# Kernel optimization log

Hardware: AMD Instinct MI355X
Metric: run time of the kernel (lower is better)

Reference implementation:

```python
import jax, jax.numpy as jnp
import numpy as np

B, C, L, HEADS, DK = 32, 128, 32, 8, 64  # batch, channels, lattice side (L1=L2=L), heads, head dim
NLAYER = 4


def setup_inputs() -> dict:
    key = jax.random.key(0)
    ks = jax.random.split(key, 6)
    s_in = 1.0 / float(np.sqrt(C))          # lecun-normal scale for QKV (fan_in = channels)
    s_out = 1.0 / float(np.sqrt(HEADS * DK))  # lecun-normal scale for W0 (fan_in = dk*heads)
    return {
        "x": jax.random.normal(ks[0], (B, C, L, L), jnp.float32),
        "Wq": jax.random.normal(ks[1], (HEADS * DK, C), jnp.float32) * s_in,
        "Wk": jax.random.normal(ks[2], (HEADS * DK, C), jnp.float32) * s_in,
        "Wv": jax.random.normal(ks[3], (HEADS * DK, C), jnp.float32) * s_in,
        "R": jax.random.normal(ks[4], (HEADS, L, L), jnp.float32) * 0.02,
        "W0": jax.random.normal(ks[5], (C, HEADS * DK), jnp.float32) * s_out,
    }


def get_irpe(R):
    # r[h, i, j] = R[h, (xi - xj) mod L1, (yi - yj) mod L2]  (jnp negative indexing wraps)
    heads, L1, L2 = R.shape
    a1 = jnp.arange(L1)
    a2 = jnp.arange(L2)
    dx = (a1[:, None] - a1[None, :]) % L1        # (L1, L1)
    dy = (a2[:, None] - a2[None, :]) % L2        # (L2, L2)
    bias = R[:, dx[:, None, :, None], dy[None, :, None, :]]  # (heads, L1, L2, L1, L2)
    return bias.reshape(heads, L1 * L2, L1 * L2)


def reference(x, Wq, Wk, Wv, R, W0):
    bias = get_irpe(R)                            # (heads, N, N)
    inv_layer = 1.0 / float(np.sqrt(NLAYER + 1))
    inv_sqrt_dk = 1.0 / float(np.sqrt(DK))

    def block(xs):  # xs: (C, L, L) — single sample, as in the original __call__
        xn = xs * inv_layer
        xf = xn.reshape(C, -1)                    # (C, N)
        Q = (Wq @ xf).reshape(HEADS, DK, -1)      # 1x1 conv == matmul
        K = (Wk @ xf).reshape(HEADS, DK, -1)
        V = (Wv @ xf).reshape(HEADS, DK, -1)
        dot = jnp.einsum('hdi,hdj->hij', Q, K) + bias
        alpha = jax.nn.softmax(dot * inv_sqrt_dk, axis=-1)
        att = jnp.einsum('hij,hdj->hdi', alpha, V).reshape(HEADS * DK, -1)
        return (W0 @ att).reshape(xs.shape) + xs  # residual

    return jax.vmap(block)(x)
```

## Files before the change

### kernel.cpp

```cpp
#include <hip/hip_runtime.h>


#define NB   32
#define NH   8
#define SEQ  1024
#define DKH  64
#define HDIM 512
#define CIN  128

#define SCL 0.18033688011112042f

typedef __bf16 bf16x8 __attribute__((ext_vector_type(8)));
typedef float floatx4 __attribute__((ext_vector_type(4)));
typedef unsigned short u16x8 __attribute__((ext_vector_type(8)));
typedef unsigned int uintx4 __attribute__((ext_vector_type(4)));

__device__ __forceinline__ unsigned short f2bf(float f) {
    union { float f; unsigned int u; } c; c.f = f;
    unsigned int u = c.u;
    return (unsigned short)((u + 0x7fffu + ((u >> 16) & 1u)) >> 16);
}
__device__ __forceinline__ bf16x8 ldfrag(const unsigned short* p) {
    u16x8 v = *reinterpret_cast<const u16x8*>(p);
    return __builtin_bit_cast(bf16x8, v);
}
__device__ __forceinline__ unsigned int pkbf(float a, float b) {
    unsigned int ua = __builtin_bit_cast(unsigned int, a);
    unsigned int ub = __builtin_bit_cast(unsigned int, b);
    ua += 0x7fffu + ((ua >> 16) & 1u);
    ub += 0x7fffu + ((ub >> 16) & 1u);
    return __builtin_amdgcn_perm(ub, ua, 0x07060302u);
}
__device__ __forceinline__ unsigned int pkbf_t(float a, float b) {
    return __builtin_amdgcn_perm(__builtin_bit_cast(unsigned int, b),
                                 __builtin_bit_cast(unsigned int, a), 0x07060302u);
}


__global__ __launch_bounds__(256) void prep_wb(const float* __restrict__ Wq,
                                               const float* __restrict__ Wk,
                                               const float* __restrict__ Wv,
                                               const float* __restrict__ W0,
                                               const float* __restrict__ R,
                                               unsigned short* __restrict__ w2,
                                               unsigned short* __restrict__ w0f,
                                               float* __restrict__ biasG) {
    if (blockIdx.x < 256) {
        int gidx = blockIdx.x * 256 + threadIdx.x;
        int lane = gidx & 63, slot = gidx >> 6;
        int bb = slot & 1, a = (slot >> 1) & 1, dxx = (slot >> 2) & 31, h = slot >> 7;
        int q = lane >> 4, n = lane & 15;
        int iy = (a << 4) + n;
        const float* Rh = R + (h << 10) + (dxx << 5);
        floatx4 v;
        for (int r = 0; r < 4; ++r) {
            int jy = (bb << 4) + 4 * q + r;
            v[r] = Rh[(iy - jy) & 31] * SCL;
        }
        *(floatx4*)&biasG[(size_t)gidx * 4] = v;
    } else {
        int idx = (blockIdx.x - 256) * 256 + threadIdx.x;
        if (idx < 196608) {
            int row = idx >> 7, col = idx & 127;
            float v;
            if (row < 512)       v = Wq[idx] * SCL;
            else if (row < 1024) v = Wk[idx - 65536];
            else                 v = Wv[idx - 131072];
            int rt = row >> 4, nr = row & 15, kc = col >> 5, qc = (col & 31) >> 3, jc = col & 7;
            w2[((rt * 4 + kc) * 512) + (qc * 16 + nr) * 8 + jc] = f2bf(v);
        } else {
            int idx2 = idx - 196608;
            int row = idx2 >> 9, col = idx2 & 511;
            int rt = row >> 4, nr = row & 15, kcA = col >> 5, qc = (col & 31) >> 3, jc = col & 7;
            w0f[((rt * 16 + kcA) * 512) + (qc * 16 + nr) * 8 + jc] = f2bf(W0[idx2]);
        }
    }
}

__global__ __launch_bounds__(256) void prep_xt(const float* __restrict__ x,
                                               unsigned short* __restrict__ xt2) {
    __shared__ float lds[64 * 65];
    int b = blockIdx.x, c0 = blockIdx.y * 64, p0 = blockIdx.z * 64;
    int t = threadIdx.x, tr = t >> 6, tc = t & 63;
    const float inv_layer = 0.44721359549995793f;
    for (int rr = 0; rr < 16; ++rr) {
        int cl = rr * 4 + tr;
        lds[cl * 65 + tc] = x[(b * CIN + c0 + cl) * SEQ + p0 + tc];
    }
    __syncthreads();
    for (int rr = 0; rr < 16; ++rr) {
        int pl = rr * 4 + tr;
        int pos = p0 + pl, c = c0 + tc;
        int pt = pos >> 4, np = pos & 15, kc = c >> 5, qc = (c & 31) >> 3, jc = c & 7;
        xt2[((size_t)((b * 64 + pt) * 4 + kc) * 512) + (qc * 16 + np) * 8 + jc] =
            f2bf(lds[tc * 65 + pl] * inv_layer);
    }
}

__global__ __launch_bounds__(256, 4) void qkv_gemm(const unsigned short* __restrict__ xt2,
                                                   const unsigned short* __restrict__ w2,
                                                   unsigned short* __restrict__ Qt,
                                                   unsigned short* __restrict__ Kf,
                                                   unsigned short* __restrict__ Vf) {
    int b = blockIdx.x, y = blockIdx.y, zt = blockIdx.z;
    int tid = threadIdx.x, wave = tid >> 6, lane = tid & 63, q = lane >> 4, n = lane & 15;
    floatx4 acc[4];
    for (int s = 0; s < 4; ++s) acc[s] = (floatx4){0.f, 0.f, 0.f, 0.f};
    bf16x8 af[4], bfr[4][4];
    if (y < 16) {
        int rt = y * 4 + wave;
        const unsigned short* wbase = w2 + (size_t)rt * 4 * 512 + lane * 8;
        const unsigned short* xbase = xt2 + (size_t)(b * 64 + zt * 4) * 4 * 512 + lane * 8;
        for (int kc = 0; kc < 4; ++kc) af[kc] = ldfrag(wbase + kc * 512);
        for (int s = 0; s < 4; ++s)
            for (int kc = 0; kc < 4; ++kc) bfr[s][kc] = ldfrag(xbase + (s * 4 + kc) * 512);
        for (int kc = 0; kc < 4; ++kc)
            for (int s = 0; s < 4; ++s)
                acc[s] = __builtin_amdgcn_mfma_f32_16x16x32_bf16(af[kc], bfr[s][kc], acc[s], 0, 0, 0);
        int wrow0 = y * 64 + wave * 16;
        int pos0 = zt * 64;
        if (y < 8) {
            int h = wrow0 >> 6;
            int d0 = (wrow0 & 63) + 4 * q;
            for (int s = 0; s < 4; ++s) {
                uint2 pk;
                pk.x = pkbf(acc[s][0], acc[s][1]);
                pk.y = pkbf(acc[s][2], acc[s][3]);
                int pos = pos0 + 16 * s + n;
                *(uint2*)&Qt[((size_t)(b * NH + h) * SEQ + pos) * DKH + d0] = pk;
            }
        } else {
            int h = (wrow0 >> 6) - 8;
            int bh = b * NH + h;
            int cd = wave >> 1;
            int qk = 2 * (wave & 1) + (q >> 1);
            int jk = 4 * (q & 1);
            for (int s = 0; s < 4; ++s) {
                uint2 pk;
                pk.x = pkbf(acc[s][0], acc[s][1]);
                pk.y = pkbf(acc[s][2], acc[s][3]);
                size_t addr = ((size_t)(bh * 16 + zt) * 8 + s * 2 + cd) * 512
                              + (qk * 16 + n) * 8 + jk;
                *(uint2*)&Kf[addr] = pk;
            }
        }
    } else {
        int pt = zt * 4 + wave;
        const unsigned short* xbase = xt2 + (size_t)((b * 64 + pt) * 4) * 512 + lane * 8;
        int rtv0 = 64 + (y - 16) * 4;
        const unsigned short* wbase = w2 + (size_t)rtv0 * 4 * 512 + lane * 8;
        for (int kc = 0; kc < 4; ++kc) af[kc] = ldfrag(xbase + kc * 512);
        for (int s = 0; s < 4; ++s)
            for (int kc = 0; kc < 4; ++kc) bfr[s][kc] = ldfrag(wbase + (s * 4 + kc) * 512);
        for (int kc = 0; kc < 4; ++kc)
            for (int s = 0; s < 4; ++s)
                acc[s] = __builtin_amdgcn_mfma_f32_16x16x32_bf16(af[kc], bfr[s][kc], acc[s], 0, 0, 0);
        int vrow0 = (y - 16) * 64;
        int cj = wave >> 1;
        int jj0 = 4 * (wave & 1);
        for (int s = 0; s < 4; ++s) {
            int vrow = vrow0 + 16 * s + n;
            int h = vrow >> 6, d = vrow & 63;
            int u = d >> 4, nl = d & 15;
            uint2 pk;
            pk.x = pkbf(acc[s][0], acc[s][1]);
            pk.y = pkbf(acc[s][2], acc[s][3]);
            size_t addr = ((size_t)((b * NH + h) * 16 + zt) * 8 + u * 2 + cj) * 512
                          + (q * 16 + nl) * 8 + jj0;
            *(uint2*)&Vf[addr] = pk;
        }
    }
}

__global__ __launch_bounds__(256, 2) void attn_kernel(const unsigned short* __restrict__ Qt,
                                                      const unsigned short* __restrict__ Kf,
                                                      const unsigned short* __restrict__ Vf,
                                                      const float* __restrict__ biasG,
                                                      unsigned short* __restrict__ att2) {
    __shared__ alignas(16) unsigned short lds_k[2][8 * 512];
    __shared__ alignas(16) unsigned short lds_v[2][8 * 512];

    int gid = blockIdx.x;
    int bh = gid & 255, qb = gid >> 8;
    int b = bh >> 3, h = bh & 7;
    int tid = threadIdx.x, wave = tid >> 6, lane = tid & 63, q = lane >> 4, n = lane & 15;
    int i0 = qb * 256 + wave * 64;
    int ti0 = i0 >> 4;

    const unsigned short* qbase = Qt + (size_t)bh * SEQ * DKH;
    const unsigned short* kft = Kf + (size_t)bh * 16 * 4096;
    const unsigned short* vft = Vf + (size_t)bh * 16 * 4096;
    const float* bGh = biasG + ((size_t)h * 32 * 4 * 256) + lane * 4;

    bf16x8 aq[4][2];
    for (int qt = 0; qt < 4; ++qt)
        for (int c = 0; c < 2; ++c)
            aq[qt][c] = ldfrag(qbase + (i0 + 16 * qt + n) * DKH + c * 32 + q * 8);

    u16x8 ones_u;
    for (int t = 0; t < 8; ++t) ones_u[t] = 0x3F80;
    bf16x8 vone = __builtin_bit_cast(bf16x8, ones_u);

    floatx4 o[4][4], acc_l[4];
    for (int qt = 0; qt < 4; ++qt) {
        acc_l[qt] = (floatx4){0.f, 0.f, 0.f, 0.f};
        for (int u = 0; u < 4; ++u) o[qt][u] = (floatx4){0.f, 0.f, 0.f, 0.f};
    }

    {
        const unsigned short* kp = kft + tid * 16;
        const unsigned short* vp = vft + tid * 16;
        u16x8 k0 = *(const u16x8*)kp, k1 = *(const u16x8*)(kp + 8);
        u16x8 v0 = *(const u16x8*)vp, v1 = *(const u16x8*)(vp + 8);
        *(u16x8*)&lds_k[0][tid * 16]     = k0;
        *(u16x8*)&lds_k[0][tid * 16 + 8] = k1;
        *(u16x8*)&lds_v[0][tid * 16]     = v0;
        *(u16x8*)&lds_v[0][tid * 16 + 8] = v1;
    }
    __syncthreads();

    for (int kt = 0; kt < 16; ++kt) {
        int cur = kt & 1;
        u16x8 kpre0, kpre1, vpre0, vpre1;
        if (kt < 15) {
            const unsigned short* kp = kft + (kt + 1) * 4096 + tid * 16;
            const unsigned short* vp = vft + (kt + 1) * 4096 + tid * 16;
            kpre0 = *(const u16x8*)kp;  kpre1 = *(const u16x8*)(kp + 8);
            vpre0 = *(const u16x8*)vp;  vpre1 = *(const u16x8*)(vp + 8);
        }

        floatx4 bsv[4][4];
        for (int qt = 0; qt < 4; ++qt) {
            int tq = ti0 + qt;
            int a512 = (tq & 1) << 9;
            int e0 = (tq >> 1) - 2 * kt;
            for (int s = 0; s < 4; ++s) {
                int dxx = (e0 - (s >> 1)) & 31;
                bsv[qt][s] = *(const floatx4*)(bGh + (dxx << 10) + a512 + ((s & 1) << 8));
            }
        }

        bf16x8 kf2[4][2];
        for (int s = 0; s < 4; ++s)
            for (int c = 0; c < 2; ++c)
                kf2[s][c] = ldfrag(&lds_k[cur][(s * 2 + c) * 512 + lane * 8]);

        bf16x8 pf[4][2];
        for (int qt = 0; qt < 4; ++qt) {
            floatx4 sv[4];
            for (int s = 0; s < 4; ++s) {
                sv[s] = __builtin_amdgcn_mfma_f32_16x16x32_bf16(kf2[s][0], aq[qt][0], bsv[qt][s], 0, 0, 0);
                sv[s] = __builtin_amdgcn_mfma_f32_16x16x32_bf16(kf2[s][1], aq[qt][1], sv[s], 0, 0, 0);
            }
            for (int c = 0; c < 2; ++c) {
                uintx4 pu;
                pu[0] = pkbf_t(__builtin_amdgcn_exp2f(sv[2 * c][0]), __builtin_amdgcn_exp2f(sv[2 * c][1]));
                pu[1] = pkbf_t(__builtin_amdgcn_exp2f(sv[2 * c][2]), __builtin_amdgcn_exp2f(sv[2 * c][3]));
                pu[2] = pkbf_t(__builtin_amdgcn_exp2f(sv[2 * c + 1][0]), __builtin_amdgcn_exp2f(sv[2 * c + 1][1]));
                pu[3] = pkbf_t(__builtin_amdgcn_exp2f(sv[2 * c + 1][2]), __builtin_amdgcn_exp2f(sv[2 * c + 1][3]));
                pf[qt][c] = __builtin_bit_cast(bf16x8, pu);
            }
        }

        bf16x8 vf2[4][2];
        for (int u = 0; u < 4; ++u)
            for (int c = 0; c < 2; ++c)
                vf2[u][c] = ldfrag(&lds_v[cur][(u * 2 + c) * 512 + lane * 8]);
        for (int qt = 0; qt < 4; ++qt) {
            acc_l[qt] = __builtin_amdgcn_mfma_f32_16x16x32_bf16(vone, pf[qt][0], acc_l[qt], 0, 0, 0);
            acc_l[qt] = __builtin_amdgcn_mfma_f32_16x16x32_bf16(vone, pf[qt][1], acc_l[qt], 0, 0, 0);
        }
        for (int u = 0; u < 4; ++u)
            for (int qt = 0; qt < 4; ++qt) {
                o[qt][u] = __builtin_amdgcn_mfma_f32_16x16x32_bf16(vf2[u][0], pf[qt][0], o[qt][u], 0, 0, 0);
                o[qt][u] = __builtin_amdgcn_mfma_f32_16x16x32_bf16(vf2[u][1], pf[qt][1], o[qt][u], 0, 0, 0);
            }

        if (kt < 15) {
            int nxt = cur ^ 1;
            *(u16x8*)&lds_k[nxt][tid * 16]     = kpre0;
            *(u16x8*)&lds_k[nxt][tid * 16 + 8] = kpre1;
            *(u16x8*)&lds_v[nxt][tid * 16]     = vpre0;
            *(u16x8*)&lds_v[nxt][tid * 16 + 8] = vpre1;
        }
        __syncthreads();
    }

    for (int qt = 0; qt < 4; ++qt) {
        float inv = 1.0f / acc_l[qt][0];
        int pt = ti0 + qt;
        for (int u = 0; u < 4; ++u) {
            int kcA = 2 * h + (u >> 1);
            int q2 = 2 * (u & 1) + (q >> 1);
            uint2 pk;
            pk.x = pkbf(o[qt][u][0] * inv, o[qt][u][1] * inv);
            pk.y = pkbf(o[qt][u][2] * inv, o[qt][u][3] * inv);
            size_t addr = ((size_t)((b * 64 + pt) * 16 + kcA) * 512)
                          + (q2 * 16 + n) * 8 + 4 * (q & 1);
            *(uint2*)&att2[addr] = pk;
        }
    }
}

__global__ __launch_bounds__(256, 4) void out_gemm(const unsigned short* __restrict__ att2,
                                                   const unsigned short* __restrict__ w0f,
                                                   const float* __restrict__ x,
                                                   float* __restrict__ out) {
    int b = blockIdx.x, ct = blockIdx.y, ptb = blockIdx.z;
    int tid = threadIdx.x, wave = tid >> 6, lane = tid & 63, q = lane >> 4, n = lane & 15;
    int pos0 = ptb * 64 + wave * 16;
    int c0 = ct * 64;
    int pt = ptb * 4 + wave;
    const unsigned short* abase = att2 + (size_t)(b * 64 + pt) * 16 * 512 + lane * 8;
    const unsigned short* wbase = w0f + (size_t)(c0 >> 4) * 16 * 512 + lane * 8;
    floatx4 acc[4];
    for (int s = 0; s < 4; ++s) acc[s] = (floatx4){0.f, 0.f, 0.f, 0.f};
    for (int g = 0; g < 4; ++g) {
        bf16x8 af[4], bfr[4][4];
        for (int k2 = 0; k2 < 4; ++k2) af[k2] = ldfrag(abase + (g * 4 + k2) * 512);
        for (int s = 0; s < 4; ++s)
            for (int k2 = 0; k2 < 4; ++k2)
                bfr[s][k2] = ldfrag(wbase + (s * 16 + g * 4 + k2) * 512);
        for (int k2 = 0; k2 < 4; ++k2)
            for (int s = 0; s < 4; ++s)
                acc[s] = __builtin_amdgcn_mfma_f32_16x16x32_bf16(af[k2], bfr[s][k2], acc[s], 0, 0, 0);
    }
    int p0q = pos0 + 4 * q;
    for (int s = 0; s < 4; ++s) {
        int c = c0 + 16 * s + n;
        size_t idx = ((size_t)b * CIN + c) * SEQ + p0q;
        floatx4 res = *(const floatx4*)&x[idx];
        floatx4 v = acc[s] + res;
        *(floatx4*)&out[idx] = v;
    }
}

extern "C" void kernel_launch(void* const* d_in, const int* in_sizes, int n_in,
                              void* d_out, int out_size, void* d_ws, size_t ws_size,
                              hipStream_t stream) {
    const float* x  = (const float*)d_in[0];
    const float* Wq = (const float*)d_in[1];
    const float* Wk = (const float*)d_in[2];
    const float* Wv = (const float*)d_in[3];
    const float* R  = (const float*)d_in[4];
    const float* W0 = (const float*)d_in[5];
    float* out = (float*)d_out;

    char* ws = (char*)d_ws;
    size_t off = 0;
    unsigned short* Qt   = (unsigned short*)(ws + off); off += (size_t)NB * NH * SEQ * DKH * 2;
    unsigned short* Kf   = (unsigned short*)(ws + off); off += (size_t)NB * NH * SEQ * DKH * 2;
    unsigned short* Vf   = (unsigned short*)(ws + off); off += (size_t)NB * NH * SEQ * DKH * 2;
    unsigned short* att2 = (unsigned short*)(ws + off); off += (size_t)NB * SEQ * HDIM * 2;
    unsigned short* xt2  = (unsigned short*)(ws + off); off += (size_t)NB * SEQ * CIN * 2;
    unsigned short* w2   = (unsigned short*)(ws + off); off += (size_t)1536 * 128 * 2;
    unsigned short* w0f  = (unsigned short*)(ws + off); off += (size_t)128 * 512 * 2;
    float* biasG = (float*)(ws + off); off += (size_t)NH * 32 * 4 * 256 * 4;
    (void)ws_size; (void)in_sizes; (void)n_in; (void)out_size;

    prep_wb<<<1280, 256, 0, stream>>>(Wq, Wk, Wv, W0, R, w2, w0f, biasG);
    prep_xt<<<dim3(NB, 2, 16), 256, 0, stream>>>(x, xt2);
    qkv_gemm<<<dim3(NB, 24, 16), 256, 0, stream>>>(xt2, w2, Qt, Kf, Vf);
    attn_kernel<<<NB * NH * 4, 256, 0, stream>>>(Qt, Kf, Vf, biasG, att2);
    out_gemm<<<dim3(NB, 2, 16), 256, 0, stream>>>(att2, w0f, x, out);
}
```

Measured before the change: 214.5 us.

## Use direct global-to-LDS loads and halve per-block query tile in attention

The attention kernel now streams K/V tiles into shared memory with global_load_lds DMA instead of staging them through registers, and drops the register prefetch copies. Each block handles 128 queries (32 per wave) instead of 256, doubling the grid and raising the occupancy target to 4 blocks per CU. Bias values are loaded inline per tile rather than batched up front. This cuts register pressure and raises parallelism, but every K/V tile is now reloaded by twice as many blocks, and there is a possible race on the DMA completing before the barrier.

New measurement: 230.9 us. +7.6%, slower.

```diff
diff --git a/kernel.cpp b/kernel.cpp
--- a/kernel.cpp
+++ b/kernel.cpp
@@ -34,6 +34,11 @@
 __device__ __forceinline__ unsigned int pkbf_t(float a, float b) {
     return __builtin_amdgcn_perm(__builtin_bit_cast(unsigned int, b),
                                  __builtin_bit_cast(unsigned int, a), 0x07060302u);
+}
+__device__ __forceinline__ void dma16(const unsigned short* g, unsigned short* l) {
+    __builtin_amdgcn_global_load_lds(
+        (const __attribute__((address_space(1))) unsigned int*)g,
+        (__attribute__((address_space(3))) unsigned int*)l, 16, 0, 0);
 }
 
 
@@ -172,7 +177,7 @@
     }
 }
 
-__global__ __launch_bounds__(256, 2) void attn_kernel(const unsigned short* __restrict__ Qt,
+__global__ __launch_bounds__(256, 4) void attn_kernel(const unsigned short* __restrict__ Qt,
                                                       const unsigned short* __restrict__ Kf,
                                                       const unsigned short* __restrict__ Vf,
                                                       const float* __restrict__ biasG,
@@ -184,7 +189,7 @@
     int bh = gid & 255, qb = gid >> 8;
     int b = bh >> 3, h = bh & 7;
     int tid = threadIdx.x, wave = tid >> 6, lane = tid & 63, q = lane >> 4, n = lane & 15;
-    int i0 = qb * 256 + wave * 64;
+    int i0 = qb * 128 + wave * 32;
     int ti0 = i0 >> 4;
 
     const unsigned short* qbase = Qt + (size_t)bh * SEQ * DKH;
@@ -192,8 +197,8 @@
     const unsigned short* vft = Vf + (size_t)bh * 16 * 4096;
     const float* bGh = biasG + ((size_t)h * 32 * 4 * 256) + lane * 4;
 
-    bf16x8 aq[4][2];
-    for (int qt = 0; qt < 4; ++qt)
+    bf16x8 aq[2][2];
+    for (int qt = 0; qt < 2; ++qt)
         for (int c = 0; c < 2; ++c)
             aq[qt][c] = ldfrag(qbase + (i0 + 16 * qt + n) * DKH + c * 32 + q * 8);
 
@@ -201,43 +206,29 @@
     for (int t = 0; t < 8; ++t) ones_u[t] = 0x3F80;
     bf16x8 vone = __builtin_bit_cast(bf16x8, ones_u);
 
-    floatx4 o[4][4], acc_l[4];
-    for (int qt = 0; qt < 4; ++qt) {
+    floatx4 o[2][4], acc_l[2];
+    for (int qt = 0; qt < 2; ++qt) {
         acc_l[qt] = (floatx4){0.f, 0.f, 0.f, 0.f};
         for (int u = 0; u < 4; ++u) o[qt][u] = (floatx4){0.f, 0.f, 0.f, 0.f};
     }
 
-    {
-        const unsigned short* kp = kft + tid * 16;
-        const unsigned short* vp = vft + tid * 16;
-        u16x8 k0 = *(const u16x8*)kp, k1 = *(const u16x8*)(kp + 8);
-        u16x8 v0 = *(const u16x8*)vp, v1 = *(const u16x8*)(vp + 8);
-        *(u16x8*)&lds_k[0][tid * 16]     = k0;
-        *(u16x8*)&lds_k[0][tid * 16 + 8] = k1;
-        *(u16x8*)&lds_v[0][tid * 16]     = v0;
-        *(u16x8*)&lds_v[0][tid * 16 + 8] = v1;
-    }
+    int sb = wave * 1024;
+    dma16(kft + sb + lane * 8,        &lds_k[0][sb]);
+    dma16(kft + sb + 512 + lane * 8,  &lds_k[0][sb + 512]);
+    dma16(vft + sb + lane * 8,        &lds_v[0][sb]);
+    dma16(vft + sb + 512 + lane * 8,  &lds_v[0][sb + 512]);
     __syncthreads();
 
     for (int kt = 0; kt < 16; ++kt) {
         int cur = kt & 1;
-        u16x8 kpre0, kpre1, vpre0, vpre1;
         if (kt < 15) {
-            const unsigned short* kp = kft + (kt + 1) * 4096 + tid * 16;
-            const unsigned short* vp = vft + (kt + 1) * 4096 + tid * 16;
-            kpre0 = *(const u16x8*)kp;  kpre1 = *(const u16x8*)(kp + 8);
-            vpre0 = *(const u16x8*)vp;  vpre1 = *(const u16x8*)(vp + 8);
-        }
-
-        floatx4 bsv[4][4];
-        for (int qt = 0; qt < 4; ++qt) {
-            int tq = ti0 + qt;
-            int a512 = (tq & 1) << 9;
-            int e0 = (tq >> 1) - 2 * kt;
-            for (int s = 0; s < 4; ++s) {
-                int dxx = (e0 - (s >> 1)) & 31;
-                bsv[qt][s] = *(const floatx4*)(bGh + (dxx << 10) + a512 + ((s & 1) << 8));
-            }
+            int nxt = cur ^ 1;
+            const unsigned short* kp = kft + (kt + 1) * 4096 + sb;
+            const unsigned short* vp = vft + (kt + 1) * 4096 + sb;
+            dma16(kp + lane * 8,       &lds_k[nxt][sb]);
+            dma16(kp + 512 + lane * 8, &lds_k[nxt][sb + 512]);
+            dma16(vp + lane * 8,       &lds_v[nxt][sb]);
+            dma16(vp + 512 + lane * 8, &lds_v[nxt][sb + 512]);
         }
 
         bf16x8 kf2[4][2];
@@ -245,11 +236,16 @@
             for (int c = 0; c < 2; ++c)
                 kf2[s][c] = ldfrag(&lds_k[cur][(s * 2 + c) * 512 + lane * 8]);
 
-        bf16x8 pf[4][2];
-        for (int qt = 0; qt < 4; ++qt) {
+        bf16x8 pf[2][2];
+        for (int qt = 0; qt < 2; ++qt) {
+            int tq = ti0 + qt;
+            int a512 = (tq & 1) << 9;
+            int e0 = (tq >> 1) - 2 * kt;
             floatx4 sv[4];
             for (int s = 0; s < 4; ++s) {
-                sv[s] = __builtin_amdgcn_mfma_f32_16x16x32_bf16(kf2[s][0], aq[qt][0], bsv[qt][s], 0, 0, 0);
+                int dxx = (e0 - (s >> 1)) & 31;
+                floatx4 bsv = *(const floatx4*)(bGh + (dxx << 10) + a512 + ((s & 1) << 8));
+                sv[s] = __builtin_amdgcn_mfma_f32_16x16x32_bf16(kf2[s][0], aq[qt][0], bsv, 0, 0, 0);
                 sv[s] = __builtin_amdgcn_mfma_f32_16x16x32_bf16(kf2[s][1], aq[qt][1], sv[s], 0, 0, 0);
             }
             for (int c = 0; c < 2; ++c) {
@@ -266,27 +262,20 @@
         for (int u = 0; u < 4; ++u)
             for (int c = 0; c < 2; ++c)
                 vf2[u][c] = ldfrag(&lds_v[cur][(u * 2 + c) * 512 + lane * 8]);
-        for (int qt = 0; qt < 4; ++qt) {
+        for (int qt = 0; qt < 2; ++qt) {
             acc_l[qt] = __builtin_amdgcn_mfma_f32_16x16x32_bf16(vone, pf[qt][0], acc_l[qt], 0, 0, 0);
             acc_l[qt] = __builtin_amdgcn_mfma_f32_16x16x32_bf16(vone, pf[qt][1], acc_l[qt], 0, 0, 0);
         }
         for (int u = 0; u < 4; ++u)
-            for (int qt = 0; qt < 4; ++qt) {
+            for (int qt = 0; qt < 2; ++qt) {
                 o[qt][u] = __builtin_amdgcn_mfma_f32_16x16x32_bf16(vf2[u][0], pf[qt][0], o[qt][u], 0, 0, 0);
                 o[qt][u] = __builtin_amdgcn_mfma_f32_16x16x32_bf16(vf2[u][1], pf[qt][1], o[qt][u], 0, 0, 0);
             }
 
-        if (kt < 15) {
-            int nxt = cur ^ 1;
-            *(u16x8*)&lds_k[nxt][tid * 16]     = kpre0;
-            *(u16x8*)&lds_k[nxt][tid * 16 + 8] = kpre1;
-            *(u16x8*)&lds_v[nxt][tid * 16]     = vpre0;
-            *(u16x8*)&lds_v[nxt][tid * 16 + 8] = vpre1;
-        }
         __syncthreads();
     }
 
-    for (int qt = 0; qt < 4; ++qt) {
+    for (int qt = 0; qt < 2; ++qt) {
         float inv = 1.0f / acc_l[qt][0];
         int pt = ti0 + qt;
         for (int u = 0; u < 4; ++u) {
@@ -361,6 +350,6 @@
     prep_wb<<<1280, 256, 0, stream>>>(Wq, Wk, Wv, W0, R, w2, w0f, biasG);
     prep_xt<<<dim3(NB, 2, 16), 256, 0, stream>>>(x, xt2);
     qkv_gemm<<<dim3(NB, 24, 16), 256, 0, stream>>>(xt2, w2, Qt, Kf, Vf);
-    attn_kernel<<<NB * NH * 4, 256, 0, stream>>>(Qt, Kf, Vf, biasG, att2);
+    attn_kernel<<<NB * NH * 8, 256, 0, stream>>>(Qt, Kf, Vf, biasG, att2);
     out_gemm<<<dim3(NB, 2, 16), 256, 0, stream>>>(att2, w0f, x, out);
 }
```
